# Kernel tuning notes

Measured on AMD Instinct MI355X. Metric: run time of the kernel, lower is better.

The kernel has to match this reference:

```python
import jax, jax.numpy as jnp
import numpy as np

DN = ('NCWXYZ', 'OIWXYZ', 'NCWXYZ')  # 4 spatial dims W,X,Y,Z

def conv4d(x, w, b):
    # 'same' padding for kernel 3 -> pad 1 on each side of all 4 spatial dims
    y = jax.lax.conv_general_dilated(
        x, w, window_strides=(1, 1, 1, 1), padding=[(1, 1)] * 4,
        dimension_numbers=DN)
    return y + b[None, :, None, None, None, None]

def net(x, w1, b1, w2, b2, w3, b3):
    x = jax.nn.relu(conv4d(x, w1, b1))
    x = jax.nn.relu(conv4d(x, w2, b2))
    x = jax.nn.relu(conv4d(x, w3, b3))
    return x

def setup_inputs() -> dict:
    key = jax.random.key(0)
    ks = jax.random.split(key, 4)
    S = 24
    x = jax.random.normal(ks[0], (8, 1, S, S, S, S), dtype=jnp.float32)
    # Kaiming-ish scale: 1/sqrt(fan_in), fan_in = in_ch * 3^4
    w1 = jax.random.normal(ks[1], (16, 1, 3, 3, 3, 3), dtype=jnp.float32) / np.sqrt(1 * 81)
    w2 = jax.random.normal(ks[2], (16, 16, 3, 3, 3, 3), dtype=jnp.float32) / np.sqrt(16 * 81)
    w3 = jax.random.normal(ks[3], (1, 16, 3, 3, 3, 3), dtype=jnp.float32) / np.sqrt(16 * 81)
    return {
        'x': x,
        'w1': w1, 'b1': jnp.zeros((16,), jnp.float32),
        'w2': w2, 'b2': jnp.zeros((16,), jnp.float32),
        'w3': w3, 'b3': jnp.zeros((1,), jnp.float32),
    }

def reference(x, w1, b1, w2, b2, w3, b3):
    # symmetric_mode: out = f(x) + P(f(P(x))), P swaps the two spatial pairs
    p = (0, 1, 4, 5, 2, 3)
    y = net(x, w1, b1, w2, b2, w3, b3)
    ys = jnp.transpose(net(jnp.transpose(x, p), w1, b1, w2, b2, w3, b3), p)
    return y + ys
```

## Files before the change

### kernel.cpp

```cpp
#include <hip/hip_runtime.h>
#include <hip/hip_bf16.h>
#include <stdint.h>


#define S   24
#define S2  576
#define S3  13824
#define S4  331776

typedef __attribute__((ext_vector_type(8)))  short bf16x8;
typedef __attribute__((ext_vector_type(4)))  float f32x4;
typedef __attribute__((ext_vector_type(4)))  int   i32x4;

__device__ __forceinline__ uint32_t f2bf(float f) {
    uint32_t u = __float_as_uint(f);
    return (u + 0x7FFFu + ((u >> 16) & 1u)) >> 16;
}
__device__ __forceinline__ int permtap(int t) {
    int kw = t / 27, kx = (t / 9) % 3, ky = (t / 3) % 3, kz = t % 3;
    return ky * 27 + kz * 9 + kw * 3 + kx;
}

#define WP1_OFF    0
#define WP3C_OFF   10368
#define WP2F_OFF   20736
#define BUF_OFF    131072
#define Y1P_PER_BR 12460032ull
#define Y2P_IN     24920064ull
#define PER_N      49840128ull
#define WS_NEED    (BUF_OFF + PER_N)

__global__ void prep_weights(const float* __restrict__ w1, const float* __restrict__ w2,
                             const float* __restrict__ w3,
                             float* __restrict__ Wp1, ushort* __restrict__ Wp3c,
                             ushort* __restrict__ Wp2f) {
    const int bid = blockIdx.x, tid = threadIdx.x;
    if (bid < 180) {
        int i = bid * 256 + tid;
        int j = i & 7, l = (i >> 3) & 63, idx = i >> 9;
        int s = idx % 5, ph = (idx / 5) % 9, br = idx / 45;
        int tapl = 2 * s + (l >> 5);
        int co = l & 15, ci = ((l >> 4) & 1) * 8 + j;
        ushort v = 0;
        if (tapl < 9) {
            int dw = ph / 3, dx = ph % 3, dy = tapl / 3, dz = tapl % 3;
            int t = dw * 27 + dx * 9 + dy * 3 + dz;
            int ts = br ? permtap(t) : t;
            v = (ushort)f2bf(w2[(co * 16 + ci) * 81 + ts]);
        }
        Wp2f[i] = v;
    } else {
        int i = (bid - 180) * 256 + tid;
        if (i < 2592) {
            int ci = i & 15, t = (i >> 4) % 81, br = i / 1296;
            int ts = br ? permtap(t) : t;
            Wp1[i]  = w1[ci * 81 + ts];
            Wp3c[i] = (ushort)f2bf(w3[ci * 81 + ts]);
        }
    }
}

__global__ __launch_bounds__(256) void halo_zero(char* __restrict__ bufbase) {
    const int tid = threadIdx.x;
    const int pb = blockIdx.x % 576, nb = blockIdx.x / 576;
    char* buf = bufbase + (size_t)nb * PER_N;
    for (int i = tid; i < 800; i += 256) {
        int cell, part, sect;
        if (i < 400) { sect = i / 200; cell = (i % 200) >> 1; part = i & 1; }
        else         { sect = 2;       cell = (i - 400) >> 2; part = i & 3; }
        int cy, cz;
        if (cell < 26)      { cy = 0;  cz = cell; }
        else if (cell < 52) { cy = 25; cz = cell - 26; }
        else if (cell < 76) { cy = cell - 51; cz = 0; }
        else                { cy = cell - 75; cz = 25; }
        size_t rec = (size_t)pb * 676 + cy * 26 + cz;
        char* dst;
        if (sect < 2) dst = buf + (size_t)sect * Y1P_PER_BR + rec * 32 + part * 16;
        else          dst = buf + Y2P_IN + rec * 64 + part * 16;
        *(uint4*)dst = make_uint4(0u, 0u, 0u, 0u);
    }
}

__global__ __launch_bounds__(576) void conv1_plane2(
    const float* __restrict__ x_c, const float* __restrict__ Wp1g,
    const float* __restrict__ b1, char* __restrict__ bufbase) {
    __shared__ float xl[9 * 676];
    const int tid = threadIdx.x;
    const int nl = blockIdx.x / 576, pb = blockIdx.x % 576;
    const float* xn = x_c + (size_t)nl * S4;
    uint32_t* y1p0 = (uint32_t*)(bufbase + (size_t)nl * PER_N);
    const int w = pb / 24, xx = pb % 24;
    for (int g = tid; g < 6084; g += 576) {
        int wi = g / 2028, r1 = g - wi * 2028;
        int xi = r1 / 676, r2 = r1 - xi * 676;
        int yp = r2 / 26, zp = r2 - yp * 26;
        int ws_ = w + wi - 1, xs = xx + xi - 1, ys = yp - 1, zs = zp - 1;
        float v = 0.f;
        if ((unsigned)ws_ < 24u && (unsigned)xs < 24u && (unsigned)ys < 24u && (unsigned)zs < 24u)
            v = xn[((ws_ * 24 + xs) * 24 + ys) * 24 + zs];
        xl[g] = v;
    }
    __syncthreads();
    const int yy = tid / 24, zz = tid - yy * 24;
    float a0[16], a1[16];
#pragma unroll
    for (int c = 0; c < 16; ++c) { a0[c] = 0.f; a1[c] = 0.f; }
#pragma unroll 1
    for (int dw = 0; dw < 3; ++dw)
#pragma unroll 1
        for (int dx = 0; dx < 3; ++dx) {
            const float* xp = &xl[(dw * 3 + dx) * 676];
#pragma unroll
            for (int dy = 0; dy < 3; ++dy)
#pragma unroll
                for (int dz = 0; dz < 3; ++dz) {
                    float xv = xp[(yy + dy) * 26 + (zz + dz)];
                    const int t = ((dw * 3 + dx) * 3 + dy) * 3 + dz;
                    const float* wt0 = &Wp1g[t << 4];
                    const float* wt1 = &Wp1g[1296 + (t << 4)];
#pragma unroll
                    for (int c = 0; c < 16; ++c) {
                        a0[c] = fmaf(xv, wt0[c], a0[c]);
                        a1[c] = fmaf(xv, wt1[c], a1[c]);
                    }
                }
        }
    const size_t rec = (size_t)((w * 24 + xx) * 26 + yy + 1) * 26 + zz + 1;
    uint32_t pk[8];
#pragma unroll
    for (int cp = 0; cp < 8; ++cp) {
        float a = fmaxf(a0[2 * cp]     + b1[2 * cp],     0.f);
        float b = fmaxf(a0[2 * cp + 1] + b1[2 * cp + 1], 0.f);
        pk[cp] = f2bf(a) | (f2bf(b) << 16);
    }
    uint32_t* dst0 = y1p0 + rec * 8;
    *(uint4*)dst0       = make_uint4(pk[0], pk[1], pk[2], pk[3]);
    *(uint4*)(dst0 + 4) = make_uint4(pk[4], pk[5], pk[6], pk[7]);
#pragma unroll
    for (int cp = 0; cp < 8; ++cp) {
        float a = fmaxf(a1[2 * cp]     + b1[2 * cp],     0.f);
        float b = fmaxf(a1[2 * cp + 1] + b1[2 * cp + 1], 0.f);
        pk[cp] = f2bf(a) | (f2bf(b) << 16);
    }
    uint32_t* dst1 = y1p0 + (Y1P_PER_BR / 4) + rec * 8;
    *(uint4*)dst1       = make_uint4(pk[0], pk[1], pk[2], pk[3]);
    *(uint4*)(dst1 + 4) = make_uint4(pk[4], pk[5], pk[6], pk[7]);
}

#define RING_A 12480

__global__ __launch_bounds__(256) void conv2_mfma(
    const char* __restrict__ bufbase, const char* __restrict__ Wp2f0,
    const float* __restrict__ b2) {
    __shared__ char lds[2 * RING_A];
    const int tid = threadIdx.x, lane = tid & 63, wid = tid >> 6;
    const int bid = blockIdx.x, cpx = gridDim.x >> 3;
    const int wg = (bid & 7) * cpx + (bid >> 3);
    const int n = wg / 3456, rr = wg - n * 3456;
    const int br = rr / 1728, b = rr - br * 1728;
    const char* y1p = bufbase + (size_t)n * PER_N + (size_t)br * Y1P_PER_BR;
    const char* Bb = Wp2f0 + br * 46080 + lane * 16;
    ushort* y2b = (ushort*)(bufbase + (size_t)n * PER_N + Y2P_IN) + br * 16;
    const int w = b / 72, r0 = b % 72, xx = r0 / 3, y0 = (r0 % 3) * 8;

    const int h = (lane >> 4) & 1;
    const bool th = lane >= 32;
    const int pyA = (lane >> 3) & 1, pzA = lane & 7;
    int aoffs[9];
#pragma unroll
    for (int t = 0; t < 9; ++t) {
        int dy = t / 3, dz = t % 3;
        aoffs[t] = ((2 * wid + pyA + dy) * 26 + (pzA + dz)) * 48 + h * 16;
    }
    int srelA[4], dstA[4]; bool actA[4];
#pragma unroll
    for (int it = 0; it < 4; ++it) {
        int g = tid + it * 256;
        actA[it] = g < 780;
        int row = g / 3, part = g - row * 3;
        srelA[it] = row * 32 + (part & 1) * 16;
        dstA[it] = ((tid & ~63) + it * 256) * 16;
    }

    f32x4 acc[3];
#pragma unroll
    for (int m = 0; m < 3; ++m) acc[m] = f32x4{0.f, 0.f, 0.f, 0.f};

#define STAGEA(ph_, rb_) do {                                                       \
    int dw_ = (ph_) / 3, dx_ = (ph_) % 3;                                           \
    int wc_ = min(max(w + dw_ - 1, 0), 23), xc_ = min(max(xx + dx_ - 1, 0), 23);    \
    const char* inpl_ = y1p + (size_t)((wc_ * 24 + xc_) * 676 + y0 * 26) * 32;      \
    _Pragma("unroll")                                                               \
    for (int it_ = 0; it_ < 4; ++it_) {                                             \
        if (actA[it_])                                                              \
            __builtin_amdgcn_global_load_lds(                                       \
                (const __attribute__((address_space(1))) void*)(inpl_ + srelA[it_]),\
                (__attribute__((address_space(3))) void*)(lds + (rb_) + dstA[it_]), \
                16, 0, 0);                                                          \
    }                                                                               \
} while (0)

    i32x4 bcur[5], bnxt[5];
#pragma unroll
    for (int s = 0; s < 5; ++s) bcur[s] = *(const i32x4*)(Bb + s * 1024);
    STAGEA(0, 0);

    int ring = 0;
#pragma unroll 1
    for (int ph = 0; ph < 9; ++ph) {
        __syncthreads();
        if (ph < 8) {
            STAGEA(ph + 1, ring ^ RING_A);
            const char* bp = Bb + (ph + 1) * 5120;
#pragma unroll
            for (int s = 0; s < 5; ++s) bnxt[s] = *(const i32x4*)(bp + s * 1024);
        }
        const int dw = ph / 3, dx = ph % 3;
        const bool valid = ((unsigned)(w + dw - 1) < 24u) && ((unsigned)(xx + dx - 1) < 24u);
        if (valid) {
#pragma unroll
            for (int s = 0; s < 5; ++s) {
                int t0 = aoffs[2 * s];
                int t1 = aoffs[(2 * s + 1 < 9) ? (2 * s + 1) : 8];
                int asel = th ? t1 : t0;
                const char* ap = lds + ring + asel;
#pragma unroll
                for (int m = 0; m < 3; ++m) {
                    i32x4 avr = *(const i32x4*)(ap + m * 384);
                    acc[m] = __builtin_amdgcn_mfma_f32_16x16x32_bf16(
                        __builtin_bit_cast(bf16x8, avr),
                        __builtin_bit_cast(bf16x8, bcur[s]), acc[m], 0, 0, 0);
                }
            }
        }
        ring ^= RING_A;
#pragma unroll
        for (int s = 0; s < 5; ++s) bcur[s] = bnxt[s];
    }
#undef STAGEA

    const int co = lane & 15;
    const float bb = b2[co];
    const int py = (lane >> 5) & 1, c4 = ((lane >> 4) & 1) * 4;
    const size_t planeb = (size_t)(w * 24 + xx) * 676;
    const size_t rowb = planeb + (size_t)(y0 + 2 * wid + py + 1) * 26 + 1;
#pragma unroll
    for (int m = 0; m < 3; ++m)
#pragma unroll
        for (int r = 0; r < 4; ++r) {
            float v = fmaxf(acc[m][r] + bb, 0.f);
            y2b[(rowb + m * 8 + c4 + r) * 32 + co] = (ushort)f2bf(v);
        }
}

#define RING3   20800
#define W3C_LDS 41600

__global__ __launch_bounds__(256) void conv3_mfma(
    const char* __restrict__ bufbase, const char* __restrict__ Wp3c,
    const float* __restrict__ b3, float* __restrict__ out_c) {
    __shared__ char lds[2 * RING3 + 5184];
    const int tid = threadIdx.x, lane = tid & 63, wid = tid >> 6;
    const int bid = blockIdx.x, cpx = gridDim.x >> 3;
    const int wg = (bid & 7) * cpx + (bid >> 3);
    const int n = wg / 1728, r0a = wg - n * 1728;
    const char* y2p = bufbase + (size_t)n * PER_N + Y2P_IN;
    float* outn = out_c + (size_t)n * S4;
    const int w = r0a / 72, r0 = r0a % 72, xx = r0 / 3, y0 = (r0 % 3) * 8;

    const int col = lane & 15, g16 = (lane >> 4) & 3;
    const int pyA = (lane >> 3) & 1, pzA = lane & 7;
    int a3[9];
#pragma unroll
    for (int t = 0; t < 9; ++t) {
        int dy = t / 3, dz = t % 3;
        a3[t] = ((2 * wid + pyA + dy) * 26 + (pzA + dz)) * 80 + g16 * 16;
    }
    const bool bact = (col == 0 && g16 < 2) || (col == 1 && g16 >= 2);
    const int colsel = (col < 2) ? col : 0;
    const int b_base = W3C_LDS + colsel * 2592 + (g16 & 1) * 16;
    const int bmask = bact ? -1 : 0;

    int srel3[6], dst3[6]; bool act3[6];
#pragma unroll
    for (int it = 0; it < 6; ++it) {
        int g = tid + it * 256;
        int c_ = g / 5, p_ = g - c_ * 5;
        act3[it] = (g < 1300) && (p_ < 4);
        srel3[it] = c_ * 64 + p_ * 16;
        dst3[it] = ((tid & ~63) + it * 256) * 16;
    }

#pragma unroll
    for (int it = 0; it < 2; ++it) {
        int g = tid + it * 256;
        if (g < 324)
            __builtin_amdgcn_global_load_lds(
                (const __attribute__((address_space(1))) void*)(Wp3c + g * 16),
                (__attribute__((address_space(3))) void*)
                    (lds + W3C_LDS + ((tid & ~63) + it * 256) * 16),
                16, 0, 0);
    }

    f32x4 acc[3];
#pragma unroll
    for (int m = 0; m < 3; ++m) acc[m] = f32x4{0.f, 0.f, 0.f, 0.f};

#define STAGE3(ph_, rb_) do {                                                       \
    int dw_ = (ph_) / 3, dx_ = (ph_) % 3;                                           \
    int wc_ = min(max(w + dw_ - 1, 0), 23), xc_ = min(max(xx + dx_ - 1, 0), 23);    \
    const char* slab_ = y2p + (size_t)((wc_ * 24 + xc_) * 676 + y0 * 26) * 64;      \
    _Pragma("unroll")                                                               \
    for (int it_ = 0; it_ < 6; ++it_) {                                             \
        if (act3[it_])                                                              \
            __builtin_amdgcn_global_load_lds(                                       \
                (const __attribute__((address_space(1))) void*)(slab_ + srel3[it_]),\
                (__attribute__((address_space(3))) void*)(lds + (rb_) + dst3[it_]), \
                16, 0, 0);                                                          \
    }                                                                               \
} while (0)

    STAGE3(0, 0);
    int ring = 0;
#pragma unroll 1
    for (int ph = 0; ph < 9; ++ph) {
        __syncthreads();
        if (ph < 8) STAGE3(ph + 1, ring ^ RING3);
        int dw = ph / 3, dx = ph % 3;
        bool valid = ((unsigned)(w + dw - 1) < 24u) && ((unsigned)(xx + dx - 1) < 24u);
        if (valid) {
#pragma unroll
            for (int tl = 0; tl < 9; ++tl) {
                int tap = ph * 9 + tl;
                i32x4 braw = *(const i32x4*)(lds + b_base + tap * 32);
                i32x4 bm;
                bm[0] = braw[0] & bmask; bm[1] = braw[1] & bmask;
                bm[2] = braw[2] & bmask; bm[3] = braw[3] & bmask;
#pragma unroll
                for (int m = 0; m < 3; ++m) {
                    i32x4 avr = *(const i32x4*)(lds + ring + a3[tl] + m * 640);
                    acc[m] = __builtin_amdgcn_mfma_f32_16x16x32_bf16(
                        __builtin_bit_cast(bf16x8, avr),
                        __builtin_bit_cast(bf16x8, bm), acc[m], 0, 0, 0);
                }
            }
        }
        ring ^= RING3;
    }
#undef STAGE3

    const float bv = b3[0];
    const int py = (lane >> 5) & 1, c4 = ((lane >> 4) & 1) * 4;
    const int yo = y0 + 2 * wid + py;
    float* obase = outn + ((size_t)(w * 24 + xx) * 24 + yo) * 24;
#pragma unroll
    for (int m = 0; m < 3; ++m) {
        float o[4];
#pragma unroll
        for (int r = 0; r < 4; ++r) {
            float mine = acc[m][r];
            float oth = __shfl_xor(mine, 1);
            o[r] = fmaxf(mine + bv, 0.f) + fmaxf(oth + bv, 0.f);
        }
        if (col == 0)
            *(float4*)(obase + m * 8 + c4) = make_float4(o[0], o[1], o[2], o[3]);
    }
}

extern "C" void kernel_launch(void* const* d_in, const int* in_sizes, int n_in,
                              void* d_out, int out_size, void* d_ws, size_t ws_size,
                              hipStream_t stream) {
    const float* x  = (const float*)d_in[0];
    const float* w1 = (const float*)d_in[1];
    const float* b1 = (const float*)d_in[2];
    const float* w2 = (const float*)d_in[3];
    const float* b2 = (const float*)d_in[4];
    const float* w3 = (const float*)d_in[5];
    const float* b3 = (const float*)d_in[6];
    float* out = (float*)d_out;
    char* ws = (char*)d_ws;
    if (ws_size < WS_NEED) return;

    float*  Wp1  = (float*)(ws + WP1_OFF);
    ushort* Wp3c = (ushort*)(ws + WP3C_OFF);
    ushort* Wp2f = (ushort*)(ws + WP2F_OFF);
    char* bufbase = ws + BUF_OFF;

    int NB = (int)((ws_size - BUF_OFF) / PER_N);
    if (NB > 8) NB = 8;
    if (NB < 1) return;
    const int nchunks = (8 + NB - 1) / NB;
    const int base = 8 / nchunks, rem = 8 % nchunks;

    prep_weights<<<191, 256, 0, stream>>>(w1, w2, w3, Wp1, Wp3c, Wp2f);
    halo_zero<<<NB * 576, 256, 0, stream>>>(bufbase);

    int c = 0;
    for (int k = 0; k < nchunks; ++k) {
        const int nb = base + (k < rem ? 1 : 0);
        conv1_plane2<<<nb * 576, 576, 0, stream>>>(
            x + (size_t)c * S4, Wp1, b1, bufbase);
        conv2_mfma<<<nb * 3456, 256, 0, stream>>>(
            bufbase, (const char*)Wp2f, b2);
        conv3_mfma<<<nb * 1728, 256, 0, stream>>>(
            bufbase, (const char*)Wp3c, b3, out + (size_t)c * S4);
        c += nb;
    }
}
```

Baseline: 845.1 us.

## Switch conv2 to 32x32x16 MFMA with parity-split LDS layout and z-pair weight tiling

Conv2 is rewritten to use 32x32x16 bf16 MFMA instructions. Each wave computes 24 output positions across two adjacent z columns using 12 per-phase weight slabs, and the staged activations are stored in LDS split into even and odd z parity. The weight prep builds a larger transposed, zero-padded weight tensor, and B fragments are now loaded from global memory each phase instead of being double-buffered in registers. Conv3 drops its LDS copy of the weights and reads them from global memory per phase. The aim is fewer MFMA issues and LDS reads per output, at the cost of extra zero-padded MACs (12 slabs per phase instead of 9 taps, 24 of 32 rows used) and possible global-load latency on the weight reads.

```diff
diff --git a/kernel.cpp b/kernel.cpp
--- a/kernel.cpp
+++ b/kernel.cpp
@@ -10,6 +10,7 @@
 
 typedef __attribute__((ext_vector_type(8)))  short bf16x8;
 typedef __attribute__((ext_vector_type(4)))  float f32x4;
+typedef __attribute__((ext_vector_type(16))) float f32x16;
 typedef __attribute__((ext_vector_type(4)))  int   i32x4;
 
 __device__ __forceinline__ uint32_t f2bf(float f) {
@@ -23,8 +24,8 @@
 
 #define WP1_OFF    0
 #define WP3C_OFF   10368
-#define WP2F_OFF   20736
-#define BUF_OFF    131072
+#define WP2T_OFF   16384
+#define BUF_OFF    262144
 #define Y1P_PER_BR 12460032ull
 #define Y2P_IN     24920064ull
 #define PER_N      49840128ull
@@ -33,24 +34,25 @@
 __global__ void prep_weights(const float* __restrict__ w1, const float* __restrict__ w2,
                              const float* __restrict__ w3,
                              float* __restrict__ Wp1, ushort* __restrict__ Wp3c,
-                             ushort* __restrict__ Wp2f) {
+                             ushort* __restrict__ Wp2T) {
     const int bid = blockIdx.x, tid = threadIdx.x;
-    if (bid < 180) {
+    if (bid < 432) {
         int i = bid * 256 + tid;
-        int j = i & 7, l = (i >> 3) & 63, idx = i >> 9;
-        int s = idx % 5, ph = (idx / 5) % 9, br = idx / 45;
-        int tapl = 2 * s + (l >> 5);
-        int co = l & 15, ci = ((l >> 4) & 1) * 8 + j;
+        int j = i & 7, lane = (i >> 3) & 63, rest = i >> 9;
+        int a = rest % 12, ph = (rest / 12) % 9, br = rest / 108;
+        int col = lane & 31, co = col & 15, s = col >> 4;
+        int ci = (lane >> 5) * 8 + j;
+        int dy = a >> 2, dzA = a & 3, dz = dzA - s;
         ushort v = 0;
-        if (tapl < 9) {
-            int dw = ph / 3, dx = ph % 3, dy = tapl / 3, dz = tapl % 3;
+        if (dz >= 0 && dz <= 2) {
+            int dw = ph / 3, dx = ph % 3;
             int t = dw * 27 + dx * 9 + dy * 3 + dz;
             int ts = br ? permtap(t) : t;
             v = (ushort)f2bf(w2[(co * 16 + ci) * 81 + ts]);
         }
-        Wp2f[i] = v;
+        Wp2T[i] = v;
     } else {
-        int i = (bid - 180) * 256 + tid;
+        int i = (bid - 432) * 256 + tid;
         if (i < 2592) {
             int ci = i & 15, t = (i >> 4) % 81, br = i / 1296;
             int ts = br ? permtap(t) : t;
@@ -101,7 +103,7 @@
         xl[g] = v;
     }
     __syncthreads();
-    const int yy = tid / 24, zz = tid - yy * 24;
+    const int yy = tid / 24, zz = tid - (tid / 24) * 24;
     float a0[16], a1[16];
 #pragma unroll
     for (int c = 0; c < 16; ++c) { a0[c] = 0.f; a1[c] = 0.f; }
@@ -149,8 +151,8 @@
 
 #define RING_A 12480
 
-__global__ __launch_bounds__(256) void conv2_mfma(
-    const char* __restrict__ bufbase, const char* __restrict__ Wp2f0,
+__global__ __launch_bounds__(256) void conv2_mfma6(
+    const char* __restrict__ bufbase, const char* __restrict__ Wp2T,
     const float* __restrict__ b2) {
     __shared__ char lds[2 * RING_A];
     const int tid = threadIdx.x, lane = tid & 63, wid = tid >> 6;
@@ -159,32 +161,37 @@
     const int n = wg / 3456, rr = wg - n * 3456;
     const int br = rr / 1728, b = rr - br * 1728;
     const char* y1p = bufbase + (size_t)n * PER_N + (size_t)br * Y1P_PER_BR;
-    const char* Bb = Wp2f0 + br * 46080 + lane * 16;
+    const char* Bb = Wp2T + (size_t)br * 110592 + lane * 16;
     ushort* y2b = (ushort*)(bufbase + (size_t)n * PER_N + Y2P_IN) + br * 16;
     const int w = b / 72, r0 = b % 72, xx = r0 / 3, y0 = (r0 % 3) * 8;
 
-    const int h = (lane >> 4) & 1;
-    const bool th = lane >= 32;
-    const int pyA = (lane >> 3) & 1, pzA = lane & 7;
-    int aoffs[9];
-#pragma unroll
-    for (int t = 0; t < 9; ++t) {
-        int dy = t / 3, dz = t % 3;
-        aoffs[t] = ((2 * wid + pyA + dy) * 26 + (pzA + dz)) * 48 + h * 16;
+    const int row = lane & 31, khalf = lane >> 5;
+    const int p_raw = wid * 24 + row;
+    const int p = (p_raw < 96) ? p_raw : 95;
+    const int y_r = p / 12, zer = (p - y_r * 12) * 2;
+    int aoff[12];
+#pragma unroll
+    for (int a = 0; a < 12; ++a) {
+        int dy = a >> 2, dzA = a & 3;
+        int zp = zer + dzA, par = zp & 1, zq = zp >> 1;
+        aoff[a] = par * 6240 + ((y_r + dy) * 13 + zq) * 48 + khalf * 16;
     }
     int srelA[4], dstA[4]; bool actA[4];
 #pragma unroll
     for (int it = 0; it < 4; ++it) {
         int g = tid + it * 256;
         actA[it] = g < 780;
-        int row = g / 3, part = g - row * 3;
-        srelA[it] = row * 32 + (part & 1) * 16;
+        int cell = g / 3, part = g - cell * 3;
+        int par_ = cell / 130, rem = cell - par_ * 130;
+        int yl = rem / 13, zq = rem - yl * 13;
+        int zp = zq * 2 + par_;
+        srelA[it] = (yl * 26 + zp) * 32 + (part & 1) * 16;
         dstA[it] = ((tid & ~63) + it * 256) * 16;
     }
 
-    f32x4 acc[3];
-#pragma unroll
-    for (int m = 0; m < 3; ++m) acc[m] = f32x4{0.f, 0.f, 0.f, 0.f};
+    f32x16 acc;
+#pragma unroll
+    for (int r = 0; r < 16; ++r) acc[r] = 0.f;
 
 #define STAGEA(ph_, rb_) do {                                                       \
     int dw_ = (ph_) / 3, dx_ = (ph_) % 3;                                           \
@@ -200,66 +207,54 @@
     }                                                                               \
 } while (0)
 
-    i32x4 bcur[5], bnxt[5];
-#pragma unroll
-    for (int s = 0; s < 5; ++s) bcur[s] = *(const i32x4*)(Bb + s * 1024);
     STAGEA(0, 0);
-
     int ring = 0;
 #pragma unroll 1
     for (int ph = 0; ph < 9; ++ph) {
         __syncthreads();
-        if (ph < 8) {
-            STAGEA(ph + 1, ring ^ RING_A);
-            const char* bp = Bb + (ph + 1) * 5120;
-#pragma unroll
-            for (int s = 0; s < 5; ++s) bnxt[s] = *(const i32x4*)(bp + s * 1024);
-        }
+        if (ph < 8) STAGEA(ph + 1, ring ^ RING_A);
+        const char* bp = Bb + ph * 12288;
+        i32x4 bf[12];
+#pragma unroll
+        for (int a = 0; a < 12; ++a)
+            bf[a] = *(const i32x4*)(bp + a * 1024);
         const int dw = ph / 3, dx = ph % 3;
         const bool valid = ((unsigned)(w + dw - 1) < 24u) && ((unsigned)(xx + dx - 1) < 24u);
         if (valid) {
 #pragma unroll
-            for (int s = 0; s < 5; ++s) {
-                int t0 = aoffs[2 * s];
-                int t1 = aoffs[(2 * s + 1 < 9) ? (2 * s + 1) : 8];
-                int asel = th ? t1 : t0;
-                const char* ap = lds + ring + asel;
-#pragma unroll
-                for (int m = 0; m < 3; ++m) {
-                    i32x4 avr = *(const i32x4*)(ap + m * 384);
-                    acc[m] = __builtin_amdgcn_mfma_f32_16x16x32_bf16(
-                        __builtin_bit_cast(bf16x8, avr),
-                        __builtin_bit_cast(bf16x8, bcur[s]), acc[m], 0, 0, 0);
-                }
+            for (int a = 0; a < 12; ++a) {
+                i32x4 avr = *(const i32x4*)(lds + ring + aoff[a]);
+                acc = __builtin_amdgcn_mfma_f32_32x32x16_bf16(
+                    __builtin_bit_cast(bf16x8, avr),
+                    __builtin_bit_cast(bf16x8, bf[a]), acc, 0, 0, 0);
             }
         }
         ring ^= RING_A;
-#pragma unroll
-        for (int s = 0; s < 5; ++s) bcur[s] = bnxt[s];
     }
 #undef STAGEA
 
-    const int co = lane & 15;
+    const int co = lane & 15, s = (lane >> 4) & 1;
     const float bb = b2[co];
-    const int py = (lane >> 5) & 1, c4 = ((lane >> 4) & 1) * 4;
-    const size_t planeb = (size_t)(w * 24 + xx) * 676;
-    const size_t rowb = planeb + (size_t)(y0 + 2 * wid + py + 1) * 26 + 1;
-#pragma unroll
-    for (int m = 0; m < 3; ++m)
-#pragma unroll
-        for (int r = 0; r < 4; ++r) {
-            float v = fmaxf(acc[m][r] + bb, 0.f);
-            y2b[(rowb + m * 8 + c4 + r) * 32 + co] = (ushort)f2bf(v);
-        }
+    const int plane676 = (w * 24 + xx) * 676;
+#pragma unroll
+    for (int r = 0; r < 16; ++r) {
+        int Drow = (r & 3) + 8 * (r >> 2) + 4 * khalf;
+        if (Drow < 24) {
+            int anc = wid * 24 + Drow;
+            int yo = anc / 12, ze = (anc - yo * 12) * 2;
+            float v = fmaxf(acc[r] + bb, 0.f);
+            y2b[(size_t)(plane676 + (y0 + yo + 1) * 26 + (ze + s + 1)) * 32 + co] =
+                (ushort)f2bf(v);
+        }
+    }
 }
 
 #define RING3   20800
-#define W3C_LDS 41600
 
 __global__ __launch_bounds__(256) void conv3_mfma(
     const char* __restrict__ bufbase, const char* __restrict__ Wp3c,
     const float* __restrict__ b3, float* __restrict__ out_c) {
-    __shared__ char lds[2 * RING3 + 5184];
+    __shared__ char lds[2 * RING3];
     const int tid = threadIdx.x, lane = tid & 63, wid = tid >> 6;
     const int bid = blockIdx.x, cpx = gridDim.x >> 3;
     const int wg = (bid & 7) * cpx + (bid >> 3);
@@ -278,7 +273,7 @@
     }
     const bool bact = (col == 0 && g16 < 2) || (col == 1 && g16 >= 2);
     const int colsel = (col < 2) ? col : 0;
-    const int b_base = W3C_LDS + colsel * 2592 + (g16 & 1) * 16;
+    const char* W3g = Wp3c + colsel * 2592 + (g16 & 1) * 16;
     const int bmask = bact ? -1 : 0;
 
     int srel3[6], dst3[6]; bool act3[6];
@@ -289,17 +284,6 @@
         act3[it] = (g < 1300) && (p_ < 4);
         srel3[it] = c_ * 64 + p_ * 16;
         dst3[it] = ((tid & ~63) + it * 256) * 16;
-    }
-
-#pragma unroll
-    for (int it = 0; it < 2; ++it) {
-        int g = tid + it * 256;
-        if (g < 324)
-            __builtin_amdgcn_global_load_lds(
-                (const __attribute__((address_space(1))) void*)(Wp3c + g * 16),
-                (__attribute__((address_space(3))) void*)
-                    (lds + W3C_LDS + ((tid & ~63) + it * 256) * 16),
-                16, 0, 0);
     }
 
     f32x4 acc[3];
@@ -326,16 +310,18 @@
     for (int ph = 0; ph < 9; ++ph) {
         __syncthreads();
         if (ph < 8) STAGE3(ph + 1, ring ^ RING3);
+        i32x4 b9[9];
+#pragma unroll
+        for (int tl = 0; tl < 9; ++tl)
+            b9[tl] = *(const i32x4*)(W3g + (ph * 9 + tl) * 32);
         int dw = ph / 3, dx = ph % 3;
         bool valid = ((unsigned)(w + dw - 1) < 24u) && ((unsigned)(xx + dx - 1) < 24u);
         if (valid) {
 #pragma unroll
             for (int tl = 0; tl < 9; ++tl) {
-                int tap = ph * 9 + tl;
-                i32x4 braw = *(const i32x4*)(lds + b_base + tap * 32);
                 i32x4 bm;
-                bm[0] = braw[0] & bmask; bm[1] = braw[1] & bmask;
-                bm[2] = braw[2] & bmask; bm[3] = braw[3] & bmask;
+                bm[0] = b9[tl][0] & bmask; bm[1] = b9[tl][1] & bmask;
+                bm[2] = b9[tl][2] & bmask; bm[3] = b9[tl][3] & bmask;
 #pragma unroll
                 for (int m = 0; m < 3; ++m) {
                     i32x4 avr = *(const i32x4*)(lds + ring + a3[tl] + m * 640);
@@ -383,7 +369,7 @@
 
     float*  Wp1  = (float*)(ws + WP1_OFF);
     ushort* Wp3c = (ushort*)(ws + WP3C_OFF);
-    ushort* Wp2f = (ushort*)(ws + WP2F_OFF);
+    ushort* Wp2T = (ushort*)(ws + WP2T_OFF);
     char* bufbase = ws + BUF_OFF;
 
     int NB = (int)((ws_size - BUF_OFF) / PER_N);
@@ -392,7 +378,7 @@
     const int nchunks = (8 + NB - 1) / NB;
     const int base = 8 / nchunks, rem = 8 % nchunks;
 
-    prep_weights<<<191, 256, 0, stream>>>(w1, w2, w3, Wp1, Wp3c, Wp2f);
+    prep_weights<<<444, 256, 0, stream>>>(w1, w2, w3, Wp1, Wp3c, Wp2T);
     halo_zero<<<NB * 576, 256, 0, stream>>>(bufbase);
 
     int c = 0;
@@ -400,8 +386,8 @@
         const int nb = base + (k < rem ? 1 : 0);
         conv1_plane2<<<nb * 576, 576, 0, stream>>>(
             x + (size_t)c * S4, Wp1, b1, bufbase);
-        conv2_mfma<<<nb * 3456, 256, 0, stream>>>(
-            bufbase, (const char*)Wp2f, b2);
+        conv2_mfma6<<<nb * 3456, 256, 0, stream>>>(
+            bufbase, (const char*)Wp2T, b2);
         conv3_mfma<<<nb * 1728, 256, 0, stream>>>(
             bufbase, (const char*)Wp3c, b3, out + (size_t)c * S4);
         c += nb;
```

New measurement: 976.3 us. +15.5%, slower.
